# Optimization experiments

Measured on AMD Instinct MI355X. Metric: run time of the kernel, lower is better.

## Reference

```python
import jax, jax.numpy as jnp
import numpy as np

B, C, H, W = 32, 384, 56, 56
WS, SS, NH = 7, 3, 12
N = WS * WS
HID = 4 * C
HD = C // NH
SCALE = HD ** -0.5
NW = (H // WS) * (W // WS)


def _rel_pos_index():
    coords = np.stack(np.meshgrid(np.arange(WS), np.arange(WS), indexing='ij'))  # 2,WS,WS
    cf = coords.reshape(2, -1)
    rel = cf[:, :, None] - cf[:, None, :]  # 2,N,N
    rel = rel.transpose(1, 2, 0).copy()
    rel[:, :, 0] += WS - 1
    rel[:, :, 1] += WS - 1
    rel[:, :, 0] *= 2 * WS - 1
    return rel.sum(-1)  # N,N int


def _win_part_np(x):
    b, h, w, c = x.shape
    x = x.reshape(b, h // WS, WS, w // WS, WS, c).transpose(0, 1, 3, 2, 4, 5)
    return x.reshape(-1, WS, WS, c)


def _attn_mask():
    img = np.zeros((1, H, W, 1), np.float32)
    cnt = 0
    for hs in (slice(0, -WS), slice(-WS, -SS), slice(-SS, None)):
        for ws_ in (slice(0, -WS), slice(-WS, -SS), slice(-SS, None)):
            img[:, hs, ws_, :] = cnt
            cnt += 1
    mw = _win_part_np(img).reshape(-1, N)
    d = mw[:, None, :] - mw[:, :, None]
    return np.where(d != 0, np.float32(-100.0), np.float32(0.0))  # nW,N,N


RPI = jnp.asarray(_rel_pos_index().reshape(-1))
MASK = jnp.asarray(_attn_mask())


def window_partition(x):
    b = x.shape[0]
    x = x.reshape(b, H // WS, WS, W // WS, WS, C).transpose(0, 1, 3, 2, 4, 5)
    return x.reshape(-1, N, C)


def window_reverse(w):
    x = w.reshape(B, H // WS, W // WS, WS, WS, C).transpose(0, 1, 3, 2, 4, 5)
    return x.reshape(B, H, W, C)


def layernorm(x, g, b, eps=1e-5):
    m = x.mean(-1, keepdims=True)
    v = jnp.mean((x - m) ** 2, -1, keepdims=True)
    return (x - m) * jax.lax.rsqrt(v + eps) * g + b


def setup_inputs():
    key = jax.random.key(0)
    ks = jax.random.split(key, 8)
    s = lambda d: 1.0 / np.sqrt(d)
    return {
        'x': jax.random.normal(ks[0], (B, C, H, W), jnp.float32),
        'qkv_w': jax.random.normal(ks[1], (C, 3 * C), jnp.float32) * s(C),
        'qkv_b': jnp.zeros((3 * C,), jnp.float32),
        'proj_w': jax.random.normal(ks[2], (C, C), jnp.float32) * s(C),
        'proj_b': jnp.zeros((C,), jnp.float32),
        'rpb_table': jax.random.normal(ks[3], ((2 * WS - 1) ** 2, NH), jnp.float32) * 0.02,
        'norm1_w': jnp.ones((C,), jnp.float32),
        'norm1_b': jnp.zeros((C,), jnp.float32),
        'norm2_w': jnp.ones((C,), jnp.float32),
        'norm2_b': jnp.zeros((C,), jnp.float32),
        'fc1_w': jax.random.normal(ks[4], (C, HID), jnp.float32) * s(C),
        'fc1_b': jnp.zeros((HID,), jnp.float32),
        'fc2_w': jax.random.normal(ks[5], (HID, C), jnp.float32) * s(HID),
        'fc2_b': jnp.zeros((C,), jnp.float32),
    }


def reference(x, qkv_w, qkv_b, proj_w, proj_b, rpb_table, norm1_w, norm1_b,
              norm2_w, norm2_b, fc1_w, fc1_b, fc2_w, fc2_b):
    x_perm = x.transpose(0, 2, 3, 1)  # B,H,W,C
    shortcut = x_perm
    shifted = jnp.roll(x_perm, (-SS, -SS), axis=(1, 2))
    xw = window_partition(shifted)  # (B*nW, N, C)
    xw = layernorm(xw, norm1_w, norm1_b)
    qkv = (xw @ qkv_w + qkv_b).reshape(-1, N, 3, NH, HD).transpose(2, 0, 3, 1, 4)
    q, k, v = qkv[0] * SCALE, qkv[1], qkv[2]  # (B*nW, NH, N, HD)
    attn = jnp.einsum('whnd,whmd->whnm', q, k)
    bias = rpb_table[RPI].reshape(N, N, NH).transpose(2, 0, 1)  # NH,N,N
    attn = attn + bias[None]
    attn = attn.reshape(B, NW, NH, N, N) + MASK[None, :, None]
    attn = jax.nn.softmax(attn.reshape(-1, NH, N, N), axis=-1)
    out = jnp.einsum('whnm,whmd->whnd', attn, v).transpose(0, 2, 1, 3).reshape(-1, N, C)
    out = out @ proj_w + proj_b
    shifted_back = window_reverse(out.reshape(-1, WS, WS, C))
    x_perm = jnp.roll(shifted_back, (SS, SS), axis=(1, 2)) + shortcut
    xn = layernorm(x_perm.reshape(B, H * W, C), norm2_w, norm2_b)
    mlp = jax.nn.gelu(xn @ fc1_w + fc1_b, approximate=False) @ fc2_w + fc2_b
    x_perm = x_perm + mlp.reshape(B, H, W, C)
    return x_perm.transpose(0, 3, 1, 2)
```

## Files before the change

### kernel.cpp

```cpp
#include <hip/hip_runtime.h>
#include <cstddef>

#define B_   32
#define C_   384
#define HW_  3136
#define NTOK 100352
#define NWIN 2048
#define NH_  12
#define SCALE_ 0.17677669529663687f

typedef __attribute__((ext_vector_type(8))) short bf16x8;
typedef __attribute__((ext_vector_type(4))) float f32x4;

__device__ __forceinline__ unsigned short f2bf(float f) {
    unsigned int u = __builtin_bit_cast(unsigned int, f);
    u = (u + 0x7FFFu + ((u >> 16) & 1u)) >> 16;
    return (unsigned short)u;
}
__device__ __forceinline__ float bf2f(unsigned short h) {
    unsigned int u = ((unsigned int)h) << 16;
    return __builtin_bit_cast(float, u);
}

__global__ __launch_bounds__(256) void k_wt(const float* __restrict__ W,
                                            unsigned short* __restrict__ Wt,
                                            int K, int N) {
    int idx = blockIdx.x * 256 + threadIdx.x;
    if (idx >= N * K) return;
    int n = idx / K, k = idx - n * K;
    Wt[idx] = f2bf(W[(size_t)k * N + n]);
}

__global__ __launch_bounds__(256) void k_meanvar(const float* __restrict__ x,
                                                 float* __restrict__ mean,
                                                 float* __restrict__ rstd) {
    int p = blockIdx.x * 256 + threadIdx.x;
    int b = p / HW_, hw = p - b * HW_;
    const float* xp = x + (size_t)b * C_ * HW_ + hw;
    float s = 0.f, sq = 0.f;
    for (int c = 0; c < C_; ++c) { float v = xp[(size_t)c * HW_]; s += v; sq += v * v; }
    float m = s * (1.0f / C_);
    float var = sq * (1.0f / C_) - m * m;
    mean[p] = m;
    rstd[p] = rsqrtf(var + 1e-5f);
}

__global__ __launch_bounds__(256) void k_ln1_gather(const float* __restrict__ x,
        const float* __restrict__ mean, const float* __restrict__ rstd,
        const float* __restrict__ g1, const float* __restrict__ b1,
        unsigned short* __restrict__ xw, unsigned short* __restrict__ xs) {
    __shared__ float T[32][33];
    int b = blockIdx.z, hw0 = blockIdx.y * 32, c0 = blockIdx.x * 32;
    int tid = threadIdx.x, lo = tid & 31, hi = tid >> 5;
    #pragma unroll
    for (int p = 0; p < 4; ++p) {
        int cr = hi + p * 8;
        T[cr][lo] = x[((size_t)b * C_ + c0 + cr) * HW_ + hw0 + lo];
    }
    __syncthreads();
    #pragma unroll
    for (int p = 0; p < 4; ++p) {
        int row = hi + p * 8;
        int hw = hw0 + row;
        int hs = hw / 56, wsrc = hw - hs * 56;
        int h = hs + 53; if (h >= 56) h -= 56;
        int w = wsrc + 53; if (w >= 56) w -= 56;
        size_t t1 = ((size_t)b * 64 + (h / 7) * 8 + (w / 7)) * 49 + (h % 7) * 7 + (w % 7);
        float m = mean[b * HW_ + hw], rs = rstd[b * HW_ + hw];
        int c = c0 + lo;
        float v = T[lo][row];
        xw[t1 * C_ + c] = f2bf((v - m) * rs * g1[c] + b1[c]);
        xs[t1 * C_ + c] = f2bf(v);
    }
}

__global__ __launch_bounds__(256) void k_gemm(const unsigned short* __restrict__ A,
        const unsigned short* __restrict__ Bt, const float* __restrict__ bias,
        unsigned short* __restrict__ out, int M, int N, int K, int mode,
        unsigned short* __restrict__ vo) {
    __shared__ unsigned short As[128][40];
    __shared__ unsigned short Bs[128][40];
    int tid = threadIdx.x;
    int lane = tid & 63, wave = tid >> 6;
    int l15 = lane & 15, quad = lane >> 4;
    int wr = wave >> 1, wc = wave & 1;
    size_t mt = blockIdx.y, nt = blockIdx.x;
    int srow = tid >> 2, scol = (tid & 3) * 8;
    const unsigned short* Ab = A + mt * 128 * (size_t)K;
    const unsigned short* Bb = Bt + nt * 128 * (size_t)K;
    f32x4 z = {0.f, 0.f, 0.f, 0.f};
    f32x4 acc[4][4];
    #pragma unroll
    for (int i = 0; i < 4; ++i)
        #pragma unroll
        for (int j = 0; j < 4; ++j) acc[i][j] = z;

    for (int k0 = 0; k0 < K; k0 += 32) {
        *(uint4*)&As[srow][scol]    = *(const uint4*)(Ab + (size_t)srow * K + k0 + scol);
        *(uint4*)&As[srow+64][scol] = *(const uint4*)(Ab + (size_t)(srow+64) * K + k0 + scol);
        *(uint4*)&Bs[srow][scol]    = *(const uint4*)(Bb + (size_t)srow * K + k0 + scol);
        *(uint4*)&Bs[srow+64][scol] = *(const uint4*)(Bb + (size_t)(srow+64) * K + k0 + scol);
        __syncthreads();
        bf16x8 af[4], bfr[4];
        #pragma unroll
        for (int mi = 0; mi < 4; ++mi) af[mi] = *(const bf16x8*)&As[wr*64 + mi*16 + l15][quad*8];
        #pragma unroll
        for (int ni = 0; ni < 4; ++ni) bfr[ni] = *(const bf16x8*)&Bs[wc*64 + ni*16 + l15][quad*8];
        #pragma unroll
        for (int mi = 0; mi < 4; ++mi)
            #pragma unroll
            for (int ni = 0; ni < 4; ++ni)
                acc[mi][ni] = __builtin_amdgcn_mfma_f32_16x16x32_bf16(af[mi], bfr[ni], acc[mi][ni], 0, 0, 0);
        __syncthreads();
    }

    int mb = (int)mt * 128 + wr * 64, nb = (int)nt * 128 + wc * 64;
    #pragma unroll
    for (int mi = 0; mi < 4; ++mi)
        #pragma unroll
        for (int ni = 0; ni < 4; ++ni) {
            int gc = nb + ni * 16 + l15;
            float bv = bias[gc];
            #pragma unroll
            for (int r = 0; r < 4; ++r) {
                int gr = mb + mi * 16 + quad * 4 + r;
                float v = acc[mi][ni][r] + bv;
                if (mode == 0) {
                    out[(size_t)gr * N + gc] = f2bf(v);
                } else if (mode == 1) {
                    v = 0.5f * v * (1.0f + erff(v * 0.70710678118654752f));
                    out[(size_t)gr * N + gc] = f2bf(v);
                } else {
                    if (gc < 768) {
                        out[(size_t)gr * 768 + gc] = f2bf(v);
                    } else {
                        int rem = gc - 768;
                        int head = rem >> 5, hd = rem & 31;
                        int win = gr / 49, tok = gr - win * 49;
                        vo[(((size_t)win * NH_ + head) * 32 + hd) * 64 + tok] = f2bf(v);
                    }
                }
            }
        }
}

__global__ __launch_bounds__(256) void k_attn(const unsigned short* __restrict__ qk,
        const unsigned short* __restrict__ vtb, const float* __restrict__ rpb,
        unsigned short* __restrict__ o) {
    __shared__ unsigned short P[4][64][72];
    int tid = threadIdx.x;
    int wave = tid >> 6, lane = tid & 63, l15 = lane & 15, quad = lane >> 4;
    int win = blockIdx.x / 3;
    int head = (blockIdx.x % 3) * 4 + wave;
    int wi = win & 63, wh = wi >> 3, ww = wi & 7;
    const unsigned short* qh = qk + (size_t)win * 49 * 768 + head * 32;
    const unsigned short* kh = qh + 384;
    const unsigned short* vh = vtb + ((size_t)win * NH_ + head) * (32 * 64);

    bf16x8 qf[4], kf[4];
    #pragma unroll
    for (int mi = 0; mi < 4; ++mi) qf[mi] = *(const bf16x8*)(qh + (size_t)(mi * 16 + l15) * 768 + quad * 8);
    #pragma unroll
    for (int ni = 0; ni < 4; ++ni) kf[ni] = *(const bf16x8*)(kh + (size_t)(ni * 16 + l15) * 768 + quad * 8);

    f32x4 z = {0.f, 0.f, 0.f, 0.f};
    f32x4 s[4][4];
    #pragma unroll
    for (int mi = 0; mi < 4; ++mi)
        #pragma unroll
        for (int ni = 0; ni < 4; ++ni)
            s[mi][ni] = __builtin_amdgcn_mfma_f32_16x16x32_bf16(qf[mi], kf[ni], z, 0, 0, 0);

    #pragma unroll
    for (int mi = 0; mi < 4; ++mi)
        #pragma unroll
        for (int r = 0; r < 4; ++r) {
            int qr = mi * 16 + quad * 4 + r;
            int qi = qr / 7, qj = qr - qi * 7;
            int rqh = (wh == 7) ? (qi < 4 ? 1 : 2) : 0;
            int rqw = (ww == 7) ? (qj < 4 ? 1 : 2) : 0;
            #pragma unroll
            for (int ni = 0; ni < 4; ++ni) {
                int kcol = ni * 16 + l15;
                float v = s[mi][ni][r] * SCALE_;
                if (qr < 49 && kcol < 49) {
                    int ki = kcol / 7, kj = kcol - ki * 7;
                    int idx = (qi - ki + 6) * 13 + (qj - kj + 6);
                    v += rpb[idx * NH_ + head];
                    int rkh = (wh == 7) ? (ki < 4 ? 1 : 2) : 0;
                    int rkw = (ww == 7) ? (kj < 4 ? 1 : 2) : 0;
                    if ((rqh * 3 + rqw) != (rkh * 3 + rkw)) v -= 100.0f;
                } else v = -1e30f;
                s[mi][ni][r] = v;
            }
        }

    float rinv[4][4];
    #pragma unroll
    for (int mi = 0; mi < 4; ++mi)
        #pragma unroll
        for (int r = 0; r < 4; ++r) {
            float m = fmaxf(fmaxf(s[mi][0][r], s[mi][1][r]), fmaxf(s[mi][2][r], s[mi][3][r]));
            #pragma unroll
            for (int d = 1; d < 16; d <<= 1) m = fmaxf(m, __shfl_xor(m, d));
            float sum = 0.f;
            #pragma unroll
            for (int ni = 0; ni < 4; ++ni) {
                float p = __expf(s[mi][ni][r] - m);
                s[mi][ni][r] = p;
                sum += p;
            }
            #pragma unroll
            for (int d = 1; d < 16; d <<= 1) sum += __shfl_xor(sum, d);
            rinv[mi][r] = 1.0f / sum;
        }

    #pragma unroll
    for (int mi = 0; mi < 4; ++mi)
        #pragma unroll
        for (int ni = 0; ni < 4; ++ni)
            #pragma unroll
            for (int r = 0; r < 4; ++r)
                P[wave][mi * 16 + quad * 4 + r][ni * 16 + l15] = f2bf(s[mi][ni][r]);
    __syncthreads();

    f32x4 oacc[4][2];
    #pragma unroll
    for (int mi = 0; mi < 4; ++mi) { oacc[mi][0] = z; oacc[mi][1] = z; }
    #pragma unroll
    for (int kt = 0; kt < 2; ++kt) {
        bf16x8 vf[2];
        #pragma unroll
        for (int n2 = 0; n2 < 2; ++n2)
            vf[n2] = *(const bf16x8*)(vh + (n2 * 16 + l15) * 64 + kt * 32 + quad * 8);
        #pragma unroll
        for (int mi = 0; mi < 4; ++mi) {
            bf16x8 pf = *(const bf16x8*)&P[wave][mi * 16 + l15][kt * 32 + quad * 8];
            #pragma unroll
            for (int n2 = 0; n2 < 2; ++n2)
                oacc[mi][n2] = __builtin_amdgcn_mfma_f32_16x16x32_bf16(pf, vf[n2], oacc[mi][n2], 0, 0, 0);
        }
    }

    #pragma unroll
    for (int mi = 0; mi < 4; ++mi)
        #pragma unroll
        for (int r = 0; r < 4; ++r) {
            int qr = mi * 16 + quad * 4 + r;
            if (qr < 49) {
                float sc = rinv[mi][r];
                #pragma unroll
                for (int n2 = 0; n2 < 2; ++n2)
                    o[((size_t)win * 49 + qr) * C_ + head * 32 + n2 * 16 + l15] =
                        f2bf(oacc[mi][n2][r] * sc);
            }
        }
}

__global__ __launch_bounds__(256) void k_resid_ln2(const unsigned short* __restrict__ proj,
        const unsigned short* __restrict__ xs, const float* __restrict__ g2,
        const float* __restrict__ b2, unsigned short* __restrict__ xn2) {
    int wave = threadIdx.x >> 6, lane = threadIdx.x & 63;
    size_t t = (size_t)blockIdx.x * 4 + wave;
    const unsigned short* pp = proj + t * C_;
    const unsigned short* sp = xs + t * C_;
    float v[6];
    float sum = 0.f, sq = 0.f;
    #pragma unroll
    for (int j = 0; j < 6; ++j) {
        int c = j * 64 + lane;
        float val = bf2f(pp[c]) + bf2f(sp[c]);
        v[j] = val; sum += val; sq += val * val;
    }
    #pragma unroll
    for (int d = 1; d < 64; d <<= 1) { sum += __shfl_xor(sum, d); sq += __shfl_xor(sq, d); }
    float m = sum * (1.0f / C_);
    float rs = rsqrtf(sq * (1.0f / C_) - m * m + 1e-5f);
    #pragma unroll
    for (int j = 0; j < 6; ++j) {
        int c = j * 64 + lane;
        xn2[t * C_ + c] = f2bf((v[j] - m) * rs * g2[c] + b2[c]);
    }
}

__global__ __launch_bounds__(256) void k_final(const unsigned short* __restrict__ xs,
        const unsigned short* __restrict__ prj, const unsigned short* __restrict__ mlp,
        float* __restrict__ out) {
    __shared__ float T[32][33];
    int b = blockIdx.z, hw0 = blockIdx.y * 32, c0 = blockIdx.x * 32;
    int tid = threadIdx.x, lo = tid & 31, hi = tid >> 5;
    #pragma unroll
    for (int p = 0; p < 4; ++p) {
        int row = hi + p * 8;
        int hw = hw0 + row;
        int ho = hw / 56, wo = hw - ho * 56;
        int h = ho + 53; if (h >= 56) h -= 56;
        int w = wo + 53; if (w >= 56) w -= 56;
        size_t t1 = ((size_t)b * 64 + (h / 7) * 8 + (w / 7)) * 49 + (h % 7) * 7 + (w % 7);
        int c = c0 + lo;
        T[row][lo] = bf2f(xs[t1 * C_ + c]) + bf2f(prj[t1 * C_ + c]) + bf2f(mlp[t1 * C_ + c]);
    }
    __syncthreads();
    #pragma unroll
    for (int p = 0; p < 4; ++p) {
        int cr = hi + p * 8;
        out[((size_t)b * C_ + c0 + cr) * HW_ + hw0 + lo] = T[lo][cr];
    }
}

extern "C" void kernel_launch(void* const* d_in, const int* in_sizes, int n_in,
                              void* d_out, int out_size, void* d_ws, size_t ws_size,
                              hipStream_t stream) {
    const float* x      = (const float*)d_in[0];
    const float* qkv_w  = (const float*)d_in[1];
    const float* qkv_b  = (const float*)d_in[2];
    const float* proj_w = (const float*)d_in[3];
    const float* proj_b = (const float*)d_in[4];
    const float* rpb    = (const float*)d_in[5];
    const float* n1w    = (const float*)d_in[6];
    const float* n1b    = (const float*)d_in[7];
    const float* n2w    = (const float*)d_in[8];
    const float* n2b    = (const float*)d_in[9];
    const float* fc1w   = (const float*)d_in[10];
    const float* fc1b   = (const float*)d_in[11];
    const float* fc2w   = (const float*)d_in[12];
    const float* fc2b   = (const float*)d_in[13];
    float* out = (float*)d_out;
    (void)ws_size; (void)in_sizes; (void)n_in; (void)out_size;

    char* ws = (char*)d_ws;
    size_t off = 0;
    auto take = [&](size_t bytes) -> char* {
        char* p = ws + off;
        off = (off + bytes + 255) & ~((size_t)255);
        return p;
    };
    const size_t SZ_TC = (size_t)NTOK * C_ * 2;
    unsigned short* xs   = (unsigned short*)take(SZ_TC);
    unsigned short* bufB = (unsigned short*)take(SZ_TC);
    unsigned short* bufC = (unsigned short*)take((size_t)(NTOK + 16) * 768 * 2);
    unsigned short* bufD = (unsigned short*)take((size_t)NWIN * NH_ * 32 * 64 * 2);
    float* meanb = (float*)take((size_t)NTOK * 4);
    float* rstdb = (float*)take((size_t)NTOK * 4);
    unsigned short* wqkv = (unsigned short*)take((size_t)1152 * 384 * 2);
    unsigned short* wprj = (unsigned short*)take((size_t)384 * 384 * 2);
    unsigned short* wfc1 = (unsigned short*)take((size_t)1536 * 384 * 2);
    unsigned short* wfc2 = (unsigned short*)take((size_t)384 * 1536 * 2);

    unsigned short* xw  = bufB;
    unsigned short* ob  = bufB;
    unsigned short* hid = bufB;
    unsigned short* qkb = bufC;
    unsigned short* prj = bufC;
    unsigned short* xn2 = bufC + (SZ_TC / 2);
    unsigned short* vt  = bufD;
    unsigned short* mlp = bufD;

    k_wt<<<(1152 * 384 + 255) / 256, 256, 0, stream>>>(qkv_w, wqkv, 384, 1152);
    k_wt<<<(384 * 384 + 255) / 256, 256, 0, stream>>>(proj_w, wprj, 384, 384);
    k_wt<<<(1536 * 384 + 255) / 256, 256, 0, stream>>>(fc1w, wfc1, 384, 1536);
    k_wt<<<(384 * 1536 + 255) / 256, 256, 0, stream>>>(fc2w, wfc2, 1536, 384);

    k_meanvar<<<NTOK / 256, 256, 0, stream>>>(x, meanb, rstdb);
    k_ln1_gather<<<dim3(12, 98, 32), 256, 0, stream>>>(x, meanb, rstdb, n1w, n1b, xw, xs);

    k_gemm<<<dim3(1152 / 128, NTOK / 128), 256, 0, stream>>>(xw, wqkv, qkv_b, qkb,
            NTOK, 1152, 384, 2, vt);
    k_attn<<<NWIN * 3, 256, 0, stream>>>(qkb, vt, rpb, ob);
    k_gemm<<<dim3(384 / 128, NTOK / 128), 256, 0, stream>>>(ob, wprj, proj_b, prj,
            NTOK, 384, 384, 0, nullptr);
    k_resid_ln2<<<NTOK / 4, 256, 0, stream>>>(prj, xs, n2w, n2b, xn2);

    const int CH = NTOK / 4;
    for (int i = 0; i < 4; ++i) {
        k_gemm<<<dim3(1536 / 128, CH / 128), 256, 0, stream>>>(
                xn2 + (size_t)i * CH * 384, wfc1, fc1b, hid, CH, 1536, 384, 1, nullptr);
        k_gemm<<<dim3(384 / 128, CH / 128), 256, 0, stream>>>(
                hid, wfc2, fc2b, mlp + (size_t)i * CH * 384, CH, 384, 1536, 0, nullptr);
    }
    k_final<<<dim3(12, 98, 32), 256, 0, stream>>>(xs, prj, mlp, out);
}
```

Before: 1.679 ms.

## Fuse LN1 stats, use direct-to-LDS loads, XCD-aware tiling, staged GEMM epilogue

The change merges the mean/variance pass and the LN1 gather into one kernel that reads each 32-pixel strip once and stages it in shared memory. The GEMM now loads tiles with global_load_lds, remaps blocks so tiles sharing B are grouped per XCD, and writes outputs through shared memory as coalesced 16-byte stores, including a transposed V scatter. The residual is folded into xs inside resid_ln2, so the final kernel reads two buffers instead of three. The MLP runs in two larger chunks with a bigger hidden buffer, which needs more workspace. The GEMM loads into unpadded LDS rows, which may cause bank conflicts, and it keeps its single-buffered synchronisation.

Result: faster. 1.359 ms (-19.1%).

```diff
diff --git a/kernel.cpp b/kernel.cpp
--- a/kernel.cpp
+++ b/kernel.cpp
@@ -21,6 +21,11 @@
     unsigned int u = ((unsigned int)h) << 16;
     return __builtin_bit_cast(float, u);
 }
+__device__ __forceinline__ void gll16(const void* g, void* l) {
+    __builtin_amdgcn_global_load_lds(
+        (const __attribute__((address_space(1))) void*)g,
+        (__attribute__((address_space(3))) void*)l, 16, 0, 0);
+}
 
 __global__ __launch_bounds__(256) void k_wt(const float* __restrict__ W,
                                             unsigned short* __restrict__ Wt,
@@ -31,63 +36,88 @@
     Wt[idx] = f2bf(W[(size_t)k * N + n]);
 }
 
-__global__ __launch_bounds__(256) void k_meanvar(const float* __restrict__ x,
-                                                 float* __restrict__ mean,
-                                                 float* __restrict__ rstd) {
-    int p = blockIdx.x * 256 + threadIdx.x;
-    int b = p / HW_, hw = p - b * HW_;
-    const float* xp = x + (size_t)b * C_ * HW_ + hw;
-    float s = 0.f, sq = 0.f;
-    for (int c = 0; c < C_; ++c) { float v = xp[(size_t)c * HW_]; s += v; sq += v * v; }
-    float m = s * (1.0f / C_);
-    float var = sq * (1.0f / C_) - m * m;
-    mean[p] = m;
-    rstd[p] = rsqrtf(var + 1e-5f);
-}
-
-__global__ __launch_bounds__(256) void k_ln1_gather(const float* __restrict__ x,
-        const float* __restrict__ mean, const float* __restrict__ rstd,
+__global__ __launch_bounds__(256) void k_ln1(const float* __restrict__ x,
         const float* __restrict__ g1, const float* __restrict__ b1,
         unsigned short* __restrict__ xw, unsigned short* __restrict__ xs) {
-    __shared__ float T[32][33];
-    int b = blockIdx.z, hw0 = blockIdx.y * 32, c0 = blockIdx.x * 32;
-    int tid = threadIdx.x, lo = tid & 31, hi = tid >> 5;
-    #pragma unroll
-    for (int p = 0; p < 4; ++p) {
-        int cr = hi + p * 8;
-        T[cr][lo] = x[((size_t)b * C_ + c0 + cr) * HW_ + hw0 + lo];
-    }
-    __syncthreads();
-    #pragma unroll
-    for (int p = 0; p < 4; ++p) {
-        int row = hi + p * 8;
-        int hw = hw0 + row;
+    __shared__ float T[384 * 33];
+    __shared__ float Ps[8][32], Pq[8][32];
+    __shared__ float Ms[32], Rs[32];
+    __shared__ int T1s[32];
+    int b = blockIdx.x / 98, strip = blockIdx.x - b * 98;
+    int hw0 = strip * 32;
+    int t = threadIdx.x;
+    const float* xb = x + (size_t)b * (C_ * HW_) + hw0;
+    #pragma unroll
+    for (int j = 0; j < 48; ++j) {
+        int flat = j * 256 + t;
+        int c = flat >> 5, pix = flat & 31;
+        T[c * 33 + pix] = xb[(size_t)c * HW_ + pix];
+    }
+    __syncthreads();
+    {
+        int pix = t & 31, ch = t >> 5;
+        float s = 0.f, q = 0.f;
+        #pragma unroll
+        for (int c = ch * 48; c < ch * 48 + 48; ++c) { float v = T[c * 33 + pix]; s += v; q += v * v; }
+        Ps[ch][pix] = s; Pq[ch][pix] = q;
+    }
+    __syncthreads();
+    if (t < 32) {
+        float s = 0.f, q = 0.f;
+        #pragma unroll
+        for (int ch = 0; ch < 8; ++ch) { s += Ps[ch][t]; q += Pq[ch][t]; }
+        float m = s * (1.0f / C_);
+        Ms[t] = m;
+        Rs[t] = rsqrtf(q * (1.0f / C_) - m * m + 1e-5f);
+        int hw = hw0 + t;
         int hs = hw / 56, wsrc = hw - hs * 56;
         int h = hs + 53; if (h >= 56) h -= 56;
         int w = wsrc + 53; if (w >= 56) w -= 56;
-        size_t t1 = ((size_t)b * 64 + (h / 7) * 8 + (w / 7)) * 49 + (h % 7) * 7 + (w % 7);
-        float m = mean[b * HW_ + hw], rs = rstd[b * HW_ + hw];
-        int c = c0 + lo;
-        float v = T[lo][row];
-        xw[t1 * C_ + c] = f2bf((v - m) * rs * g1[c] + b1[c]);
-        xs[t1 * C_ + c] = f2bf(v);
+        T1s[t] = (b * 64 + (h / 7) * 8 + (w / 7)) * 49 + (h % 7) * 7 + (w % 7);
+    }
+    __syncthreads();
+    #pragma unroll
+    for (int j = 0; j < 48; ++j) {
+        int flat = j * 256 + t;
+        int pix = flat / C_, c = flat - pix * C_;
+        float v = T[c * 33 + pix];
+        size_t o = (size_t)T1s[pix] * C_ + c;
+        xw[o] = f2bf((v - Ms[pix]) * Rs[pix] * g1[c] + b1[c]);
+        xs[o] = f2bf(v);
     }
 }
 
 __global__ __launch_bounds__(256) void k_gemm(const unsigned short* __restrict__ A,
         const unsigned short* __restrict__ Bt, const float* __restrict__ bias,
-        unsigned short* __restrict__ out, int M, int N, int K, int mode,
+        unsigned short* __restrict__ out, int NT, int K, int ldout, int mode,
         unsigned short* __restrict__ vo) {
-    __shared__ unsigned short As[128][40];
-    __shared__ unsigned short Bs[128][40];
+    __shared__ unsigned short smem[17408];
+    unsigned short* As = smem;
+    unsigned short* Bs = smem + 4096;
     int tid = threadIdx.x;
     int lane = tid & 63, wave = tid >> 6;
     int l15 = lane & 15, quad = lane >> 4;
     int wr = wave >> 1, wc = wave & 1;
-    size_t mt = blockIdx.y, nt = blockIdx.x;
-    int srow = tid >> 2, scol = (tid & 3) * 8;
-    const unsigned short* Ab = A + mt * 128 * (size_t)K;
-    const unsigned short* Bb = Bt + nt * 128 * (size_t)K;
+
+    int flat = blockIdx.x;
+    int xcd = flat & 7, s = flat >> 3;
+    int nt = s % NT, mtg = s / NT;
+    int mt = mtg * 8 + xcd;
+
+    size_t K2 = (size_t)K * 2;
+    const char* Ab = (const char*)A + (size_t)mt * 128 * K2;
+    const char* Bb = (const char*)Bt + (size_t)nt * 128 * K2;
+    int r0 = wave * 32 + (lane >> 2);
+    int cb = (lane & 3) * 16;
+    const char* gA0 = Ab + (size_t)r0 * K2 + cb;
+    const char* gA1 = Ab + (size_t)(r0 + 16) * K2 + cb;
+    const char* gB0 = Bb + (size_t)r0 * K2 + cb;
+    const char* gB1 = Bb + (size_t)(r0 + 16) * K2 + cb;
+    unsigned short* lA0 = As + wave * 1024;
+    unsigned short* lA1 = As + wave * 1024 + 512;
+    unsigned short* lB0 = Bs + wave * 1024;
+    unsigned short* lB1 = Bs + wave * 1024 + 512;
+
     f32x4 z = {0.f, 0.f, 0.f, 0.f};
     f32x4 acc[4][4];
     #pragma unroll
@@ -95,17 +125,16 @@
         #pragma unroll
         for (int j = 0; j < 4; ++j) acc[i][j] = z;
 
-    for (int k0 = 0; k0 < K; k0 += 32) {
-        *(uint4*)&As[srow][scol]    = *(const uint4*)(Ab + (size_t)srow * K + k0 + scol);
-        *(uint4*)&As[srow+64][scol] = *(const uint4*)(Ab + (size_t)(srow+64) * K + k0 + scol);
-        *(uint4*)&Bs[srow][scol]    = *(const uint4*)(Bb + (size_t)srow * K + k0 + scol);
-        *(uint4*)&Bs[srow+64][scol] = *(const uint4*)(Bb + (size_t)(srow+64) * K + k0 + scol);
+    int kiters = K >> 5;
+    for (int ki = 0; ki < kiters; ++ki) {
+        gll16(gA0, lA0); gll16(gA1, lA1); gll16(gB0, lB0); gll16(gB1, lB1);
+        gA0 += 64; gA1 += 64; gB0 += 64; gB1 += 64;
         __syncthreads();
         bf16x8 af[4], bfr[4];
         #pragma unroll
-        for (int mi = 0; mi < 4; ++mi) af[mi] = *(const bf16x8*)&As[wr*64 + mi*16 + l15][quad*8];
-        #pragma unroll
-        for (int ni = 0; ni < 4; ++ni) bfr[ni] = *(const bf16x8*)&Bs[wc*64 + ni*16 + l15][quad*8];
+        for (int mi = 0; mi < 4; ++mi) af[mi] = *(const bf16x8*)(As + (wr * 64 + mi * 16 + l15) * 32 + quad * 8);
+        #pragma unroll
+        for (int ni = 0; ni < 4; ++ni) bfr[ni] = *(const bf16x8*)(Bs + (wc * 64 + ni * 16 + l15) * 32 + quad * 8);
         #pragma unroll
         for (int mi = 0; mi < 4; ++mi)
             #pragma unroll
@@ -114,34 +143,45 @@
         __syncthreads();
     }
 
-    int mb = (int)mt * 128 + wr * 64, nb = (int)nt * 128 + wc * 64;
+    int nb = nt * 128;
     #pragma unroll
     for (int mi = 0; mi < 4; ++mi)
         #pragma unroll
         for (int ni = 0; ni < 4; ++ni) {
-            int gc = nb + ni * 16 + l15;
-            float bv = bias[gc];
+            int ct = wc * 64 + ni * 16 + l15;
+            float bv = bias[nb + ct];
             #pragma unroll
             for (int r = 0; r < 4; ++r) {
-                int gr = mb + mi * 16 + quad * 4 + r;
+                int rt = wr * 64 + mi * 16 + quad * 4 + r;
                 float v = acc[mi][ni][r] + bv;
-                if (mode == 0) {
-                    out[(size_t)gr * N + gc] = f2bf(v);
-                } else if (mode == 1) {
-                    v = 0.5f * v * (1.0f + erff(v * 0.70710678118654752f));
-                    out[(size_t)gr * N + gc] = f2bf(v);
-                } else {
-                    if (gc < 768) {
-                        out[(size_t)gr * 768 + gc] = f2bf(v);
-                    } else {
-                        int rem = gc - 768;
-                        int head = rem >> 5, hd = rem & 31;
-                        int win = gr / 49, tok = gr - win * 49;
-                        vo[(((size_t)win * NH_ + head) * 32 + hd) * 64 + tok] = f2bf(v);
-                    }
-                }
+                if (mode == 1) v = 0.5f * v * (1.0f + erff(v * 0.70710678118654752f));
+                smem[rt * 136 + ct] = f2bf(v);
             }
         }
+    __syncthreads();
+
+    if (mode != 2 || nt < 6) {
+        unsigned short* ob = out + (size_t)mt * 128 * ldout + nb;
+        #pragma unroll
+        for (int j = 0; j < 8; ++j) {
+            int f16i = j * 256 + tid;
+            int r = f16i >> 4;
+            int c = (f16i & 15) * 8;
+            *(uint4*)(ob + (size_t)r * ldout + c) = *(const uint4*)(smem + r * 136 + c);
+        }
+    } else {
+        int cbase = nb - 768;
+        #pragma unroll
+        for (int j = 0; j < 64; ++j) {
+            int fl = j * 256 + tid;
+            int c = fl >> 7, r = fl & 127;
+            int gr = mt * 128 + r;
+            int win = gr / 49, tok = gr - win * 49;
+            int rem = cbase + c;
+            int head = rem >> 5, hd = rem & 31;
+            vo[(((size_t)win * NH_ + head) * 32 + hd) * 64 + tok] = smem[r * 136 + c];
+        }
+    }
 }
 
 __global__ __launch_bounds__(256) void k_attn(const unsigned short* __restrict__ qk,
@@ -164,12 +204,12 @@
     for (int ni = 0; ni < 4; ++ni) kf[ni] = *(const bf16x8*)(kh + (size_t)(ni * 16 + l15) * 768 + quad * 8);
 
     f32x4 z = {0.f, 0.f, 0.f, 0.f};
-    f32x4 s[4][4];
+    f32x4 sc_[4][4];
     #pragma unroll
     for (int mi = 0; mi < 4; ++mi)
         #pragma unroll
         for (int ni = 0; ni < 4; ++ni)
-            s[mi][ni] = __builtin_amdgcn_mfma_f32_16x16x32_bf16(qf[mi], kf[ni], z, 0, 0, 0);
+            sc_[mi][ni] = __builtin_amdgcn_mfma_f32_16x16x32_bf16(qf[mi], kf[ni], z, 0, 0, 0);
 
     #pragma unroll
     for (int mi = 0; mi < 4; ++mi)
@@ -182,7 +222,7 @@
             #pragma unroll
             for (int ni = 0; ni < 4; ++ni) {
                 int kcol = ni * 16 + l15;
-                float v = s[mi][ni][r] * SCALE_;
+                float v = sc_[mi][ni][r] * SCALE_;
                 if (qr < 49 && kcol < 49) {
                     int ki = kcol / 7, kj = kcol - ki * 7;
                     int idx = (qi - ki + 6) * 13 + (qj - kj + 6);
@@ -191,7 +231,7 @@
                     int rkw = (ww == 7) ? (kj < 4 ? 1 : 2) : 0;
                     if ((rqh * 3 + rqw) != (rkh * 3 + rkw)) v -= 100.0f;
                 } else v = -1e30f;
-                s[mi][ni][r] = v;
+                sc_[mi][ni][r] = v;
             }
         }
 
@@ -200,14 +240,14 @@
     for (int mi = 0; mi < 4; ++mi)
         #pragma unroll
         for (int r = 0; r < 4; ++r) {
-            float m = fmaxf(fmaxf(s[mi][0][r], s[mi][1][r]), fmaxf(s[mi][2][r], s[mi][3][r]));
+            float m = fmaxf(fmaxf(sc_[mi][0][r], sc_[mi][1][r]), fmaxf(sc_[mi][2][r], sc_[mi][3][r]));
             #pragma unroll
             for (int d = 1; d < 16; d <<= 1) m = fmaxf(m, __shfl_xor(m, d));
             float sum = 0.f;
             #pragma unroll
             for (int ni = 0; ni < 4; ++ni) {
-                float p = __expf(s[mi][ni][r] - m);
-                s[mi][ni][r] = p;
+                float p = __expf(sc_[mi][ni][r] - m);
+                sc_[mi][ni][r] = p;
                 sum += p;
             }
             #pragma unroll
@@ -221,7 +261,7 @@
         for (int ni = 0; ni < 4; ++ni)
             #pragma unroll
             for (int r = 0; r < 4; ++r)
-                P[wave][mi * 16 + quad * 4 + r][ni * 16 + l15] = f2bf(s[mi][ni][r]);
+                P[wave][mi * 16 + quad * 4 + r][ni * 16 + l15] = f2bf(sc_[mi][ni][r]);
     __syncthreads();
 
     f32x4 oacc[4][2];
@@ -248,22 +288,22 @@
         for (int r = 0; r < 4; ++r) {
             int qr = mi * 16 + quad * 4 + r;
             if (qr < 49) {
-                float sc = rinv[mi][r];
+                float s = rinv[mi][r];
                 #pragma unroll
                 for (int n2 = 0; n2 < 2; ++n2)
                     o[((size_t)win * 49 + qr) * C_ + head * 32 + n2 * 16 + l15] =
-                        f2bf(oacc[mi][n2][r] * sc);
+                        f2bf(oacc[mi][n2][r] * s);
             }
         }
 }
 
 __global__ __launch_bounds__(256) void k_resid_ln2(const unsigned short* __restrict__ proj,
-        const unsigned short* __restrict__ xs, const float* __restrict__ g2,
+        unsigned short* __restrict__ xs, const float* __restrict__ g2,
         const float* __restrict__ b2, unsigned short* __restrict__ xn2) {
     int wave = threadIdx.x >> 6, lane = threadIdx.x & 63;
     size_t t = (size_t)blockIdx.x * 4 + wave;
     const unsigned short* pp = proj + t * C_;
-    const unsigned short* sp = xs + t * C_;
+    unsigned short* sp = xs + t * C_;
     float v[6];
     float sum = 0.f, sq = 0.f;
     #pragma unroll
@@ -279,13 +319,13 @@
     #pragma unroll
     for (int j = 0; j < 6; ++j) {
         int c = j * 64 + lane;
+        sp[c] = f2bf(v[j]);
         xn2[t * C_ + c] = f2bf((v[j] - m) * rs * g2[c] + b2[c]);
     }
 }
 
-__global__ __launch_bounds__(256) void k_final(const unsigned short* __restrict__ xs,
-        const unsigned short* __restrict__ prj, const unsigned short* __restrict__ mlp,
-        float* __restrict__ out) {
+__global__ __launch_bounds__(256) void k_final(const unsigned short* __restrict__ resid,
+        const unsigned short* __restrict__ mlp, float* __restrict__ out) {
     __shared__ float T[32][33];
     int b = blockIdx.z, hw0 = blockIdx.y * 32, c0 = blockIdx.x * 32;
     int tid = threadIdx.x, lo = tid & 31, hi = tid >> 5;
@@ -298,7 +338,7 @@
         int w = wo + 53; if (w >= 56) w -= 56;
         size_t t1 = ((size_t)b * 64 + (h / 7) * 8 + (w / 7)) * 49 + (h % 7) * 7 + (w % 7);
         int c = c0 + lo;
-        T[row][lo] = bf2f(xs[t1 * C_ + c]) + bf2f(prj[t1 * C_ + c]) + bf2f(mlp[t1 * C_ + c]);
+        T[row][lo] = bf2f(resid[t1 * C_ + c]) + bf2f(mlp[t1 * C_ + c]);
     }
     __syncthreads();
     #pragma unroll
@@ -339,9 +379,7 @@
     unsigned short* xs   = (unsigned short*)take(SZ_TC);
     unsigned short* bufB = (unsigned short*)take(SZ_TC);
     unsigned short* bufC = (unsigned short*)take((size_t)(NTOK + 16) * 768 * 2);
-    unsigned short* bufD = (unsigned short*)take((size_t)NWIN * NH_ * 32 * 64 * 2);
-    float* meanb = (float*)take((size_t)NTOK * 4);
-    float* rstdb = (float*)take((size_t)NTOK * 4);
+    unsigned short* bufD = (unsigned short*)take((size_t)50176 * 1536 * 2);
     unsigned short* wqkv = (unsigned short*)take((size_t)1152 * 384 * 2);
     unsigned short* wprj = (unsigned short*)take((size_t)384 * 384 * 2);
     unsigned short* wfc1 = (unsigned short*)take((size_t)1536 * 384 * 2);
@@ -349,34 +387,31 @@
 
     unsigned short* xw  = bufB;
     unsigned short* ob  = bufB;
-    unsigned short* hid = bufB;
+    unsigned short* mlp = bufB;
     unsigned short* qkb = bufC;
     unsigned short* prj = bufC;
     unsigned short* xn2 = bufC + (SZ_TC / 2);
     unsigned short* vt  = bufD;
-    unsigned short* mlp = bufD;
+    unsigned short* hid = bufD;
 
     k_wt<<<(1152 * 384 + 255) / 256, 256, 0, stream>>>(qkv_w, wqkv, 384, 1152);
     k_wt<<<(384 * 384 + 255) / 256, 256, 0, stream>>>(proj_w, wprj, 384, 384);
     k_wt<<<(1536 * 384 + 255) / 256, 256, 0, stream>>>(fc1w, wfc1, 384, 1536);
     k_wt<<<(384 * 1536 + 255) / 256, 256, 0, stream>>>(fc2w, wfc2, 1536, 384);
 
-    k_meanvar<<<NTOK / 256, 256, 0, stream>>>(x, meanb, rstdb);
-    k_ln1_gather<<<dim3(12, 98, 32), 256, 0, stream>>>(x, meanb, rstdb, n1w, n1b, xw, xs);
-
-    k_gemm<<<dim3(1152 / 128, NTOK / 128), 256, 0, stream>>>(xw, wqkv, qkv_b, qkb,
-            NTOK, 1152, 384, 2, vt);
+    k_ln1<<<32 * 98, 256, 0, stream>>>(x, n1w, n1b, xw, xs);
+
+    k_gemm<<<784 * 9, 256, 0, stream>>>(xw, wqkv, qkv_b, qkb, 9, 384, 768, 2, vt);
     k_attn<<<NWIN * 3, 256, 0, stream>>>(qkb, vt, rpb, ob);
-    k_gemm<<<dim3(384 / 128, NTOK / 128), 256, 0, stream>>>(ob, wprj, proj_b, prj,
-            NTOK, 384, 384, 0, nullptr);
+    k_gemm<<<784 * 3, 256, 0, stream>>>(ob, wprj, proj_b, prj, 3, 384, 384, 0, nullptr);
     k_resid_ln2<<<NTOK / 4, 256, 0, stream>>>(prj, xs, n2w, n2b, xn2);
 
-    const int CH = NTOK / 4;
-    for (int i = 0; i < 4; ++i) {
-        k_gemm<<<dim3(1536 / 128, CH / 128), 256, 0, stream>>>(
-                xn2 + (size_t)i * CH * 384, wfc1, fc1b, hid, CH, 1536, 384, 1, nullptr);
-        k_gemm<<<dim3(384 / 128, CH / 128), 256, 0, stream>>>(
-                hid, wfc2, fc2b, mlp + (size_t)i * CH * 384, CH, 384, 1536, 0, nullptr);
-    }
-    k_final<<<dim3(12, 98, 32), 256, 0, stream>>>(xs, prj, mlp, out);
-}
+    const int CH = 50176;
+    for (int i = 0; i < 2; ++i) {
+        k_gemm<<<392 * 12, 256, 0, stream>>>(xn2 + (size_t)i * CH * 384, wfc1, fc1b,
+                hid, 12, 384, 1536, 1, nullptr);
+        k_gemm<<<392 * 3, 256, 0, stream>>>(hid, wfc2, fc2b,
+                mlp + (size_t)i * CH * 384, 3, 1536, 384, 0, nullptr);
+    }
+    k_final<<<dim3(12, 98, 32), 256, 0, stream>>>(xs, mlp, out);
+}
```
